# Kernel tuning notes

Hardware: AMD Instinct MI355X
Metric: run time of the kernel (lower is better)

Reference implementation:

```python
import jax, jax.numpy as jnp
import numpy as np

B, N, M, C = 4, 2048, 576, 512
H, KVH, D = 8, 2, 64          # heads, kv heads, head_dim
E, TOPK, F = 8, 2, 2048       # experts, top-k, expert hidden (4*C)
EPS = 1e-6
NEG = -1e9


def setup_inputs() -> dict:
    key = jax.random.key(0)
    ks = iter(jax.random.split(key, 40))
    w = lambda shape, s=0.02: jax.random.normal(next(ks), shape, jnp.float32) * s
    d = {
        'x': jax.random.normal(next(ks), (B, N, C), jnp.float32),
        'vision_features': jax.random.normal(next(ks), (B, M, C), jnp.float32),
        'ln1_g': jnp.ones((C,), jnp.float32), 'ln1_b': jnp.zeros((C,), jnp.float32),
        'ln2_g': jnp.ones((C,), jnp.float32), 'ln2_b': jnp.zeros((C,), jnp.float32),
        'ln3_g': jnp.ones((C,), jnp.float32), 'ln3_b': jnp.zeros((C,), jnp.float32),
        # self-attention (GQA): q -> C, k/v -> KVH*D
        'sa_wq': w((C, C)), 'sa_bq': jnp.zeros((C,), jnp.float32),
        'sa_wk': w((C, KVH * D)), 'sa_bk': jnp.zeros((KVH * D,), jnp.float32),
        'sa_wv': w((C, KVH * D)), 'sa_bv': jnp.zeros((KVH * D,), jnp.float32),
        'sa_wo': w((C, C)), 'sa_bo': jnp.zeros((C,), jnp.float32),
        # cross-attention (GQA)
        'ca_wq': w((C, C)), 'ca_bq': jnp.zeros((C,), jnp.float32),
        'ca_wk': w((C, KVH * D)), 'ca_bk': jnp.zeros((KVH * D,), jnp.float32),
        'ca_wv': w((C, KVH * D)), 'ca_bv': jnp.zeros((KVH * D,), jnp.float32),
        'ca_wo': w((C, C)), 'ca_bo': jnp.zeros((C,), jnp.float32),
        # MoE: router + stacked expert MLPs (C -> F -> C, GELU)
        'router_w': w((C, E)), 'router_b': jnp.zeros((E,), jnp.float32),
        'e_w1': w((E, C, F)), 'e_b1': jnp.zeros((E, F), jnp.float32),
        'e_w2': w((E, F, C)), 'e_b2': jnp.zeros((E, C), jnp.float32),
    }
    return d


def _ln(x, g, b):
    mu = jnp.mean(x, -1, keepdims=True)
    var = jnp.mean(jnp.square(x - mu), -1, keepdims=True)
    return (x - mu) * jax.lax.rsqrt(var + EPS) * g + b


def _gqa_attn(xq, ctx, wq, bq, wk, bk, wv, bv, wo, bo, causal):
    b, n, c = xq.shape
    m = ctx.shape[1]
    q = (xq @ wq + bq).reshape(b, n, H, D).transpose(0, 2, 1, 3)      # bhnd
    k = (ctx @ wk + bk).reshape(b, m, KVH, D).transpose(0, 2, 1, 3)   # bgmd
    v = (ctx @ wv + bv).reshape(b, m, KVH, D).transpose(0, 2, 1, 3)
    rep = H // KVH
    k = jnp.repeat(k, rep, axis=1)  # repeat_interleave over head dim
    v = jnp.repeat(v, rep, axis=1)
    scores = jnp.einsum('bhnd,bhmd->bhnm', q, k) * (D ** -0.5)
    if causal:
        mask = jnp.tril(jnp.ones((n, m), bool))
        scores = jnp.where(mask, scores, NEG)
    a = jax.nn.softmax(scores, axis=-1)
    o = jnp.einsum('bhnm,bhmd->bhnd', a, v).transpose(0, 2, 1, 3).reshape(b, n, c)
    return o @ wo + bo


def _moe(x, router_w, router_b, e_w1, e_b1, e_w2, e_b2):
    logits = x @ router_w + router_b                    # [B,N,E]
    probs = jax.nn.softmax(logits, axis=-1)
    topv, topi = jax.lax.top_k(probs, TOPK)             # [B,N,K]
    topv = topv / jnp.sum(topv, -1, keepdims=True)      # renormalize top-k gates
    onehot = jax.nn.one_hot(topi, E, dtype=x.dtype)     # [B,N,K,E]
    gates = jnp.einsum('bnke,bnk->bne', onehot, topv)   # sparse gates, zeros off top-k
    h = jax.nn.gelu(jnp.einsum('bnc,ecf->bnef', x, e_w1) + e_b1)
    eo = jnp.einsum('bnef,efc->bnec', h, e_w2) + e_b2
    out = jnp.einsum('bne,bnec->bnc', gates, eo)
    # load-balance aux loss (Switch-style): E * sum_e f_e * P_e
    dispatch = jnp.sum(onehot, axis=2)                  # [B,N,E] routed mask
    f = jnp.mean(dispatch, axis=(0, 1))
    P = jnp.mean(probs, axis=(0, 1))
    aux = E * jnp.sum(f * P)
    return out, aux


def reference(x, vision_features,
              ln1_g, ln1_b, ln2_g, ln2_b, ln3_g, ln3_b,
              sa_wq, sa_bq, sa_wk, sa_bk, sa_wv, sa_bv, sa_wo, sa_bo,
              ca_wq, ca_bq, ca_wk, ca_bk, ca_wv, ca_bv, ca_wo, ca_bo,
              router_w, router_b, e_w1, e_b1, e_w2, e_b2):
    # pre-norm causal self-attn + residual
    h = _ln(x, ln1_g, ln1_b)
    x = x + _gqa_attn(h, h, sa_wq, sa_bq, sa_wk, sa_bk, sa_wv, sa_bv, sa_wo, sa_bo, True)
    # pre-norm cross-attn + residual
    h = _ln(x, ln2_g, ln2_b)
    x = x + _gqa_attn(h, vision_features, ca_wq, ca_bq, ca_wk, ca_bk, ca_wv, ca_bv, ca_wo, ca_bo, False)
    # pre-norm MoE FFN + residual
    h = _ln(x, ln3_g, ln3_b)
    m, aux = _moe(h, router_w, router_b, e_w1, e_b1, e_w2, e_b2)
    return x + m, aux
```

## Files before the change

kernel.cpp:

```cpp
#include <hip/hip_runtime.h>
#include <cstddef>
#include <cstdint>

#define B_   4
#define N_   2048
#define M_   576
#define C_   512
#define H_   8
#define KVH_ 2
#define D_   64
#define E_   8
#define F_   2048
#define BN_  (B_*N_)
#define BM_  (B_*M_)

typedef __attribute__((ext_vector_type(8))) short bf16x8;
typedef __attribute__((ext_vector_type(4))) float f32x4;

__device__ __forceinline__ unsigned short f2bf(float f) {
    union { float f; unsigned int u; } v; v.f = f;
    unsigned int r = v.u + 0x7FFFu + ((v.u >> 16) & 1u);
    return (unsigned short)(r >> 16);
}

__global__ __launch_bounds__(256) void ln_kernel(const float* __restrict__ x,
    const float* __restrict__ g, const float* __restrict__ b, float* __restrict__ out)
{
    int row = blockIdx.x;
    const float* xr = x + (size_t)row * C_;
    float s = 0.f, ss = 0.f;
    for (int c = threadIdx.x; c < C_; c += 256) { float v = xr[c]; s += v; ss += v * v; }
    __shared__ float S1[256], S2[256];
    S1[threadIdx.x] = s; S2[threadIdx.x] = ss;
    __syncthreads();
    for (int o = 128; o > 0; o >>= 1) {
        if (threadIdx.x < o) { S1[threadIdx.x] += S1[threadIdx.x + o]; S2[threadIdx.x] += S2[threadIdx.x + o]; }
        __syncthreads();
    }
    float mu  = S1[0] * (1.f / C_);
    float var = S2[0] * (1.f / C_) - mu * mu;
    float inv = rsqrtf(var + 1e-6f);
    float* orow = out + (size_t)row * C_;
    for (int c = threadIdx.x; c < C_; c += 256)
        orow[c] = (xr[c] - mu) * inv * g[c] + b[c];
}

__global__ __launch_bounds__(256) void ln_bf(const float* __restrict__ x,
    const float* __restrict__ g, const float* __restrict__ b, unsigned short* __restrict__ out)
{
    int row = blockIdx.x;
    const float* xr = x + (size_t)row * C_;
    float s = 0.f, ss = 0.f;
    for (int c = threadIdx.x; c < C_; c += 256) { float v = xr[c]; s += v; ss += v * v; }
    __shared__ float S1[256], S2[256];
    S1[threadIdx.x] = s; S2[threadIdx.x] = ss;
    __syncthreads();
    for (int o = 128; o > 0; o >>= 1) {
        if (threadIdx.x < o) { S1[threadIdx.x] += S1[threadIdx.x + o]; S2[threadIdx.x] += S2[threadIdx.x + o]; }
        __syncthreads();
    }
    float mu  = S1[0] * (1.f / C_);
    float var = S2[0] * (1.f / C_) - mu * mu;
    float inv = rsqrtf(var + 1e-6f);
    unsigned short* orow = out + (size_t)row * C_;
    for (int c = threadIdx.x; c < C_; c += 256)
        orow[c] = f2bf((xr[c] - mu) * inv * g[c] + b[c]);
}

__global__ __launch_bounds__(256) void cast_bf_kernel(const float* __restrict__ in,
    unsigned short* __restrict__ out)
{
    int i = (blockIdx.x * 256 + threadIdx.x) * 4;
    float4 v = *(const float4*)(in + i);
    ushort4 o;
    o.x = f2bf(v.x); o.y = f2bf(v.y); o.z = f2bf(v.z); o.w = f2bf(v.w);
    *(ushort4*)(out + i) = o;
}

__global__ __launch_bounds__(256) void transpose_cast(const float* __restrict__ Win,
    unsigned short* __restrict__ Wtout, int K, int N)
{
    const float* W = Win + (size_t)blockIdx.z * K * N;
    unsigned short* Wt = Wtout + (size_t)blockIdx.z * K * N;
    __shared__ float T[32][33];
    int tid = threadIdx.x;
    int r = tid >> 3, c4 = (tid & 7) * 4;
    int k0 = blockIdx.y * 32, n0 = blockIdx.x * 32;
    float4 v = *(const float4*)&W[(size_t)(k0 + r) * N + n0 + c4];
    T[r][c4 + 0] = v.x; T[r][c4 + 1] = v.y; T[r][c4 + 2] = v.z; T[r][c4 + 3] = v.w;
    __syncthreads();
    ushort4 o;
    o.x = f2bf(T[c4 + 0][r]); o.y = f2bf(T[c4 + 1][r]);
    o.z = f2bf(T[c4 + 2][r]); o.w = f2bf(T[c4 + 3][r]);
    *(ushort4*)&Wt[(size_t)(n0 + r) * K + k0 + c4] = o;
}

__global__ __launch_bounds__(256) void dense_mfma(
    const unsigned short* __restrict__ Abf,
    const unsigned short* __restrict__ Btbf,
    const float* __restrict__ bias,
    float* __restrict__ outF,
    unsigned short* __restrict__ outBf,
    int N, int K, int mode, int NkPer)
{
    int row0 = blockIdx.y * 128;
    int col0 = blockIdx.x * 128;

    __shared__ unsigned short As[128 * 40];
    __shared__ unsigned short Bs[128 * 40];

    int tid = threadIdx.x;
    int srow = tid >> 2, seg8 = (tid & 3) * 8;
    size_t abase0 = (size_t)(row0 + srow) * K;
    size_t abase1 = (size_t)(row0 + srow + 64) * K;
    size_t bbase0 = (size_t)(col0 + srow) * K;
    size_t bbase1 = (size_t)(col0 + srow + 64) * K;
    int ldsA0 = srow * 40 + seg8, ldsA1 = (srow + 64) * 40 + seg8;

    int lane = tid & 63;
    int wid = tid >> 6;
    int wm0 = (wid & 1) * 64, wn0 = (wid >> 1) * 64;
    int lm = lane & 15, lq = lane >> 4;

    int aoff[4], boff[4];
#pragma unroll
    for (int i = 0; i < 4; i++) {
        aoff[i] = (wm0 + 16 * i + lm) * 40 + lq * 8;
        boff[i] = (wn0 + 16 * i + lm) * 40 + lq * 8;
    }

    f32x4 acc[4][4];
#pragma unroll
    for (int i = 0; i < 4; i++)
#pragma unroll
        for (int j = 0; j < 4; j++)
            acc[i][j] = (f32x4){0.f, 0.f, 0.f, 0.f};

    for (int k0 = 0; k0 < K; k0 += 32) {
        __syncthreads();
        *(uint4*)&As[ldsA0] = *(const uint4*)&Abf[abase0 + k0 + seg8];
        *(uint4*)&As[ldsA1] = *(const uint4*)&Abf[abase1 + k0 + seg8];
        *(uint4*)&Bs[ldsA0] = *(const uint4*)&Btbf[bbase0 + k0 + seg8];
        *(uint4*)&Bs[ldsA1] = *(const uint4*)&Btbf[bbase1 + k0 + seg8];
        __syncthreads();

        bf16x8 av[4], bv[4];
#pragma unroll
        for (int i = 0; i < 4; i++) av[i] = *(const bf16x8*)&As[aoff[i]];
#pragma unroll
        for (int i = 0; i < 4; i++) bv[i] = *(const bf16x8*)&Bs[boff[i]];
#pragma unroll
        for (int mi = 0; mi < 4; mi++)
#pragma unroll
            for (int ni = 0; ni < 4; ni++)
                acc[mi][ni] = __builtin_amdgcn_mfma_f32_16x16x32_bf16(av[mi], bv[ni], acc[mi][ni], 0, 0, 0);
    }

#pragma unroll
    for (int mi = 0; mi < 4; mi++) {
#pragma unroll
        for (int ri = 0; ri < 4; ri++) {
            int gr = row0 + wm0 + 16 * mi + lq * 4 + ri;
            if (mode == 2) {
                int bb = gr / NkPer;
                int mm = gr - bb * NkPer;
#pragma unroll
                for (int ni = 0; ni < 4; ni++) {
                    int gc = col0 + wn0 + 16 * ni + lm;
                    outBf[((size_t)bb * (KVH_ * D_) + gc) * NkPer + mm] =
                        f2bf(acc[mi][ni][ri] + bias[gc]);
                }
            } else if (mode == 1) {
                size_t orow = (size_t)gr * N;
#pragma unroll
                for (int ni = 0; ni < 4; ni++) {
                    int gc = col0 + wn0 + 16 * ni + lm;
                    outF[orow + gc] += acc[mi][ni][ri] + bias[gc];
                }
            } else {
                size_t orow = (size_t)gr * N;
#pragma unroll
                for (int ni = 0; ni < 4; ni++) {
                    int gc = col0 + wn0 + 16 * ni + lm;
                    outBf[orow + gc] = f2bf(acc[mi][ni][ri] + bias[gc]);
                }
            }
        }
    }
}

__global__ __launch_bounds__(256) void attn_mfma(
    const unsigned short* __restrict__ Q,
    const unsigned short* __restrict__ K,
    const unsigned short* __restrict__ Vt,
    unsigned short* __restrict__ O,
    int NkPer, int causal)
{
    __shared__ unsigned short Qs[64 * 72];
    __shared__ unsigned short Ks[64 * 72];
    __shared__ unsigned short Vs[64 * 72];
    unsigned short* Ps = Qs;

    int tid = threadIdx.x;
    int qt = blockIdx.x, bh = blockIdx.y;
    int b = bh >> 3, h = bh & 7, g = h >> 2;
    int q0 = qt * 64;

#pragma unroll
    for (int i = 0; i < 2; i++) {
        int s = tid + (i << 8);
        int r = s >> 3, c8 = (s & 7) << 3;
        *(uint4*)&Qs[r * 72 + c8] =
            *(const uint4*)&Q[(size_t)(b * N_ + q0 + r) * C_ + h * D_ + c8];
    }
    __syncthreads();

    int lane = tid & 63, wid = tid >> 6;
    int lm = lane & 15, lq = lane >> 4;
    int arow = wid * 16 + lm;

    bf16x8 qf[2];
    qf[0] = *(const bf16x8*)&Qs[arow * 72 + lq * 8];
    qf[1] = *(const bf16x8*)&Qs[arow * 72 + lq * 8 + 32];

    float m_run[4], l_run[4];
    f32x4 of[4];
#pragma unroll
    for (int i = 0; i < 4; i++) { m_run[i] = -1e30f; l_run[i] = 0.f; of[i] = (f32x4){0.f,0.f,0.f,0.f}; }

    int nkt = causal ? (qt + 1) : ((NkPer + 63) >> 6);

    for (int kt = 0; kt < nkt; kt++) {
        int k0 = kt << 6;
        __syncthreads();
#pragma unroll
        for (int i = 0; i < 2; i++) {
            int s = tid + (i << 8);
            int r = s >> 3, c8 = (s & 7) << 3;
            *(uint4*)&Ks[r * 72 + c8] =
                *(const uint4*)&K[(size_t)(b * NkPer + k0 + r) * (KVH_ * D_) + g * D_ + c8];
            *(uint4*)&Vs[r * 72 + c8] =
                *(const uint4*)&Vt[(size_t)(b * (KVH_ * D_) + g * D_ + r) * NkPer + k0 + c8];
        }
        __syncthreads();

        f32x4 sf[4];
#pragma unroll
        for (int i = 0; i < 4; i++) sf[i] = (f32x4){0.f,0.f,0.f,0.f};
#pragma unroll
        for (int ks = 0; ks < 2; ks++) {
#pragma unroll
            for (int ni = 0; ni < 4; ni++) {
                bf16x8 bv = *(const bf16x8*)&Ks[(16 * ni + lm) * 72 + lq * 8 + 32 * ks];
                sf[ni] = __builtin_amdgcn_mfma_f32_16x16x32_bf16(qf[ks], bv, sf[ni], 0, 0, 0);
            }
        }

        bool diag = causal && (k0 + 63 > q0 + wid * 16);
#pragma unroll
        for (int ni = 0; ni < 4; ni++)
#pragma unroll
            for (int ri = 0; ri < 4; ri++) {
                float v = sf[ni][ri] * 0.125f;
                if (diag && (k0 + 16 * ni + lm > q0 + wid * 16 + lq * 4 + ri)) v = -1e30f;
                sf[ni][ri] = v;
            }

        float alpha[4];
#pragma unroll
        for (int ri = 0; ri < 4; ri++) {
            float mx = fmaxf(fmaxf(sf[0][ri], sf[1][ri]), fmaxf(sf[2][ri], sf[3][ri]));
            mx = fmaxf(mx, __shfl_xor(mx, 1));
            mx = fmaxf(mx, __shfl_xor(mx, 2));
            mx = fmaxf(mx, __shfl_xor(mx, 4));
            mx = fmaxf(mx, __shfl_xor(mx, 8));
            float mnew = fmaxf(m_run[ri], mx);
            float a = __expf(m_run[ri] - mnew);
            float rsum = 0.f;
#pragma unroll
            for (int ni = 0; ni < 4; ni++) {
                float p = __expf(sf[ni][ri] - mnew);
                sf[ni][ri] = p;
                rsum += p;
            }
            rsum += __shfl_xor(rsum, 1);
            rsum += __shfl_xor(rsum, 2);
            rsum += __shfl_xor(rsum, 4);
            rsum += __shfl_xor(rsum, 8);
            l_run[ri] = l_run[ri] * a + rsum;
            m_run[ri] = mnew;
            alpha[ri] = a;
        }
#pragma unroll
        for (int ni = 0; ni < 4; ni++)
#pragma unroll
            for (int ri = 0; ri < 4; ri++) of[ni][ri] *= alpha[ri];

#pragma unroll
        for (int ni = 0; ni < 4; ni++)
#pragma unroll
            for (int ri = 0; ri < 4; ri++)
                Ps[(wid * 16 + lq * 4 + ri) * 72 + 16 * ni + lm] = f2bf(sf[ni][ri]);
        __syncthreads();

        bf16x8 pf0 = *(const bf16x8*)&Ps[arow * 72 + lq * 8];
        bf16x8 pf1 = *(const bf16x8*)&Ps[arow * 72 + lq * 8 + 32];
#pragma unroll
        for (int ni = 0; ni < 4; ni++) {
            bf16x8 vv0 = *(const bf16x8*)&Vs[(16 * ni + lm) * 72 + lq * 8];
            bf16x8 vv1 = *(const bf16x8*)&Vs[(16 * ni + lm) * 72 + lq * 8 + 32];
            of[ni] = __builtin_amdgcn_mfma_f32_16x16x32_bf16(pf0, vv0, of[ni], 0, 0, 0);
            of[ni] = __builtin_amdgcn_mfma_f32_16x16x32_bf16(pf1, vv1, of[ni], 0, 0, 0);
        }
    }

#pragma unroll
    for (int ri = 0; ri < 4; ri++) {
        float inv = 1.f / l_run[ri];
        int q = q0 + wid * 16 + lq * 4 + ri;
        size_t orow = (size_t)(b * N_ + q) * C_ + h * D_;
#pragma unroll
        for (int ni = 0; ni < 4; ni++)
            O[orow + 16 * ni + lm] = f2bf(of[ni][ri] * inv);
    }
}

__global__ __launch_bounds__(256) void router_logits(const float* __restrict__ X,
    const float* __restrict__ RW, const float* __restrict__ RB,
    float* __restrict__ gprobs, int* __restrict__ topi, float* __restrict__ gatesv)
{
    int lane = threadIdx.x & 63;
    int t = blockIdx.x * 4 + (threadIdx.x >> 6);
    const float* xr = X + (size_t)t * C_;
    float p[8] = {};
    for (int i = 0; i < 8; i++) {
        int c = i * 64 + lane;
        float xv = xr[c];
#pragma unroll
        for (int e = 0; e < 8; e++) p[e] = fmaf(xv, RW[c * 8 + e], p[e]);
    }
#pragma unroll
    for (int e = 0; e < 8; e++) {
        float v = p[e];
        v += __shfl_xor(v, 32, 64);
        v += __shfl_xor(v, 16, 64);
        v += __shfl_xor(v, 8, 64);
        v += __shfl_xor(v, 4, 64);
        v += __shfl_xor(v, 2, 64);
        v += __shfl_xor(v, 1, 64);
        p[e] = v;
    }
    if (lane == 0) {
        float logits[8], mx = -1e30f;
        for (int e = 0; e < 8; e++) { logits[e] = p[e] + RB[e]; mx = fmaxf(mx, logits[e]); }
        float pr[8], sum = 0.f;
        for (int e = 0; e < 8; e++) { pr[e] = expf(logits[e] - mx); sum += pr[e]; }
        float inv = 1.f / sum;
        for (int e = 0; e < 8; e++) { pr[e] *= inv; gprobs[t * 8 + e] = pr[e]; }
        int i1 = 0;
        for (int e = 1; e < 8; e++) if (pr[e] > pr[i1]) i1 = e;
        int i2 = (i1 == 0) ? 1 : 0;
        for (int e = 0; e < 8; e++) if (e != i1 && pr[e] > pr[i2]) i2 = e;
        float v1 = pr[i1], v2 = pr[i2], sg = 1.f / (v1 + v2);
        topi[t * 2]     = i1;  topi[t * 2 + 1]   = i2;
        gatesv[t * 2]   = v1 * sg;  gatesv[t * 2 + 1] = v2 * sg;
    }
}

__global__ __launch_bounds__(256) void router_reduce(const float* __restrict__ gprobs,
    const int* __restrict__ topi, int* __restrict__ ctrl, float* __restrict__ psum)
{
    __shared__ float fs[256];
    __shared__ int   is_[256];
    int bid = blockIdx.x, tid = threadIdx.x;
    if (bid < 8) {
        float s = 0.f;
        for (int t = tid; t < BN_; t += 256) s += gprobs[t * 8 + bid];
        fs[tid] = s; __syncthreads();
        for (int o = 128; o > 0; o >>= 1) { if (tid < o) fs[tid] += fs[tid + o]; __syncthreads(); }
        if (tid == 0) psum[bid] = fs[0];
    } else {
        int e = bid - 8, c = 0;
        for (int i = tid; i < BN_ * 2; i += 256) c += (topi[i] == e);
        is_[tid] = c; __syncthreads();
        for (int o = 128; o > 0; o >>= 1) { if (tid < o) is_[tid] += is_[tid + o]; __syncthreads(); }
        if (tid == 0) ctrl[e] = is_[0];
    }
}

__global__ void router_offsets(int* __restrict__ ctrl)
{
    if (threadIdx.x == 0 && blockIdx.x == 0) {
        int off = 0;
        for (int e = 0; e < 8; e++) {
            ctrl[16 + e] = off;
            off += (ctrl[e] + 127) & ~127;
        }
        ctrl[24] = off;
    }
}

__global__ __launch_bounds__(256) void router_scatter(const int* __restrict__ topi,
    const float* __restrict__ gatesv, int* __restrict__ rowtok,
    float* __restrict__ rowgate, int* __restrict__ ctrl)
{
    __shared__ int lcnt[8];
    __shared__ int lbase[8];
    int tid = threadIdx.x;
    int t = blockIdx.x * 256 + tid;
    if (tid < 8) lcnt[tid] = 0;
    __syncthreads();
    int e0 = topi[t * 2], e1 = topi[t * 2 + 1];
    int p0 = atomicAdd(&lcnt[e0], 1);
    int p1 = atomicAdd(&lcnt[e1], 1);
    __syncthreads();
    if (tid < 8) lbase[tid] = atomicAdd(&ctrl[8 + tid], lcnt[tid]);
    __syncthreads();
    int s0 = ctrl[16 + e0] + lbase[e0] + p0;
    int s1 = ctrl[16 + e1] + lbase[e1] + p1;
    rowtok[s0] = t; rowgate[s0] = gatesv[t * 2];
    rowtok[s1] = t; rowgate[s1] = gatesv[t * 2 + 1];
}

__global__ __launch_bounds__(256) void moe_mfma(
    const unsigned short* __restrict__ Abf,
    const unsigned short* __restrict__ Btbf,
    const float* __restrict__ biasAll,
    float* __restrict__ outF,
    unsigned short* __restrict__ outBf,
    const int* __restrict__ rowtok,
    const float* __restrict__ rowgate,
    const int* __restrict__ ctrl,
    int N, int K, int mode)
{
    int e = blockIdx.z;
    int cnt = ctrl[e];
    int row0 = blockIdx.y * 128;
    if (row0 >= cnt) return;
    int off = ctrl[16 + e];
    int col0 = blockIdx.x * 128;
    const unsigned short* Bt = Btbf + (size_t)e * N * K;
    const float* bias = biasAll + (size_t)e * N;

    __shared__ unsigned short As[128 * 40];
    __shared__ unsigned short Bs[128 * 40];
    __shared__ int toks[128];

    int tid = threadIdx.x;
    if (mode == 1 && tid < 128) {
        int gl = row0 + tid;
        toks[tid] = rowtok[off + (gl < cnt ? gl : 0)];
    }
    __syncthreads();

    int srow = tid >> 2, seg8 = (tid & 3) * 8;
    size_t abase0, abase1;
    if (mode == 1) {
        abase0 = (size_t)toks[srow] * K;
        abase1 = (size_t)toks[srow + 64] * K;
    } else {
        abase0 = (size_t)(off + row0 + srow) * K;
        abase1 = (size_t)(off + row0 + srow + 64) * K;
    }
    size_t bbase0 = (size_t)(col0 + srow) * K;
    size_t bbase1 = (size_t)(col0 + srow + 64) * K;
    int ldsA0 = srow * 40 + seg8, ldsA1 = (srow + 64) * 40 + seg8;

    int lane = tid & 63;
    int wid = tid >> 6;
    int wm0 = (wid & 1) * 64, wn0 = (wid >> 1) * 64;
    int lm = lane & 15, lq = lane >> 4;

    int aoff[4], boff[4];
#pragma unroll
    for (int i = 0; i < 4; i++) {
        aoff[i] = (wm0 + 16 * i + lm) * 40 + lq * 8;
        boff[i] = (wn0 + 16 * i + lm) * 40 + lq * 8;
    }

    f32x4 acc[4][4];
#pragma unroll
    for (int i = 0; i < 4; i++)
#pragma unroll
        for (int j = 0; j < 4; j++)
            acc[i][j] = (f32x4){0.f, 0.f, 0.f, 0.f};

    for (int k0 = 0; k0 < K; k0 += 32) {
        __syncthreads();
        *(uint4*)&As[ldsA0] = *(const uint4*)&Abf[abase0 + k0 + seg8];
        *(uint4*)&As[ldsA1] = *(const uint4*)&Abf[abase1 + k0 + seg8];
        *(uint4*)&Bs[ldsA0] = *(const uint4*)&Bt[bbase0 + k0 + seg8];
        *(uint4*)&Bs[ldsA1] = *(const uint4*)&Bt[bbase1 + k0 + seg8];
        __syncthreads();

        bf16x8 av[4], bv[4];
#pragma unroll
        for (int i = 0; i < 4; i++) av[i] = *(const bf16x8*)&As[aoff[i]];
#pragma unroll
        for (int i = 0; i < 4; i++) bv[i] = *(const bf16x8*)&Bs[boff[i]];
#pragma unroll
        for (int mi = 0; mi < 4; mi++)
#pragma unroll
            for (int ni = 0; ni < 4; ni++)
                acc[mi][ni] = __builtin_amdgcn_mfma_f32_16x16x32_bf16(av[mi], bv[ni], acc[mi][ni], 0, 0, 0);
    }

#pragma unroll
    for (int mi = 0; mi < 4; mi++) {
#pragma unroll
        for (int ri = 0; ri < 4; ri++) {
            int row_l = wm0 + 16 * mi + lq * 4 + ri;
            int gl = row0 + row_l;
            if (mode == 1) {
                size_t orow = (size_t)(off + gl) * N;
#pragma unroll
                for (int ni = 0; ni < 4; ni++) {
                    int gc = col0 + wn0 + 16 * ni + lm;
                    float hv = 0.f;
                    if (gl < cnt) {
                        float xv = acc[mi][ni][ri] + bias[gc];
                        float x3 = xv * xv * xv;
                        hv = 0.5f * xv * (1.f + tanhf(0.7978845608f * (xv + 0.044715f * x3)));
                    }
                    outBf[orow + gc] = f2bf(hv);
                }
            } else {
                if (gl >= cnt) continue;
                int tok = rowtok[off + gl];
                float gt = rowgate[off + gl];
                size_t orow = (size_t)tok * N;
#pragma unroll
                for (int ni = 0; ni < 4; ni++) {
                    int gc = col0 + wn0 + 16 * ni + lm;
                    atomicAdd(&outF[orow + gc], gt * (acc[mi][ni][ri] + bias[gc]));
                }
            }
        }
    }
}

__global__ void aux_kernel(const int* __restrict__ ctrl, const float* __restrict__ psum,
                           float* __restrict__ outaux)
{
    if (threadIdx.x == 0 && blockIdx.x == 0) {
        float s = 0.f;
        for (int e = 0; e < 8; e++)
            s += ((float)ctrl[e] / (float)BN_) * (psum[e] / (float)BN_);
        outaux[0] = 8.f * s;
    }
}

extern "C" void kernel_launch(void* const* d_in, const int* in_sizes, int n_in,
                              void* d_out, int out_size, void* d_ws, size_t ws_size,
                              hipStream_t stream)
{
    const float* x      = (const float*)d_in[0];
    const float* vis    = (const float*)d_in[1];
    const float* ln1g   = (const float*)d_in[2];
    const float* ln1b   = (const float*)d_in[3];
    const float* ln2g   = (const float*)d_in[4];
    const float* ln2b   = (const float*)d_in[5];
    const float* ln3g   = (const float*)d_in[6];
    const float* ln3b   = (const float*)d_in[7];
    const float* sa_wq  = (const float*)d_in[8];
    const float* sa_bq  = (const float*)d_in[9];
    const float* sa_wk  = (const float*)d_in[10];
    const float* sa_bk  = (const float*)d_in[11];
    const float* sa_wv  = (const float*)d_in[12];
    const float* sa_bv  = (const float*)d_in[13];
    const float* sa_wo  = (const float*)d_in[14];
    const float* sa_bo  = (const float*)d_in[15];
    const float* ca_wq  = (const float*)d_in[16];
    const float* ca_bq  = (const float*)d_in[17];
    const float* ca_wk  = (const float*)d_in[18];
    const float* ca_bk  = (const float*)d_in[19];
    const float* ca_wv  = (const float*)d_in[20];
    const float* ca_bv  = (const float*)d_in[21];
    const float* ca_wo  = (const float*)d_in[22];
    const float* ca_bo  = (const float*)d_in[23];
    const float* rw     = (const float*)d_in[24];
    const float* rb     = (const float*)d_in[25];
    const float* e_w1   = (const float*)d_in[26];
    const float* e_b1   = (const float*)d_in[27];
    const float* e_w2   = (const float*)d_in[28];
    const float* e_b2   = (const float*)d_in[29];

    float* out = (float*)d_out;

    char* ws = (char*)d_ws;
    size_t off = 0;
    auto alloc = [&](size_t bytes) -> void* {
        void* p = ws + off;
        off = (off + bytes + 255) & ~(size_t)255;
        return p;
    };
    float* hbuf    = (float*)alloc((size_t)BN_ * C_ * 4);
    unsigned short* hbz = (unsigned short*)alloc((size_t)BN_ * C_ * 2);
    unsigned short* visbf = (unsigned short*)alloc((size_t)BM_ * C_ * 2);
    char* ureg = (char*)alloc((size_t)17408 * F_ * 2);
    unsigned short* moeH = (unsigned short*)ureg;
    unsigned short* qbf  = (unsigned short*)(ureg);
    unsigned short* obf  = (unsigned short*)(ureg + (size_t)BN_ * C_ * 2);
    unsigned short* kbf  = (unsigned short*)(ureg + (size_t)BN_ * C_ * 4);
    unsigned short* vtbf = (unsigned short*)(ureg + (size_t)BN_ * C_ * 4 + (size_t)BN_ * KVH_ * D_ * 2);
    unsigned short* sa_wqt = (unsigned short*)alloc((size_t)C_ * C_ * 2);
    unsigned short* sa_wkt = (unsigned short*)alloc((size_t)C_ * KVH_ * D_ * 2);
    unsigned short* sa_wvt = (unsigned short*)alloc((size_t)C_ * KVH_ * D_ * 2);
    unsigned short* sa_wot = (unsigned short*)alloc((size_t)C_ * C_ * 2);
    unsigned short* ca_wqt = (unsigned short*)alloc((size_t)C_ * C_ * 2);
    unsigned short* ca_wkt = (unsigned short*)alloc((size_t)C_ * KVH_ * D_ * 2);
    unsigned short* ca_wvt = (unsigned short*)alloc((size_t)C_ * KVH_ * D_ * 2);
    unsigned short* ca_wot = (unsigned short*)alloc((size_t)C_ * C_ * 2);
    unsigned short* w1t  = (unsigned short*)alloc((size_t)E_ * C_ * F_ * 2);
    unsigned short* w2t  = (unsigned short*)alloc((size_t)E_ * F_ * C_ * 2);
    float* gprobs  = (float*)alloc((size_t)BN_ * 8 * 4);
    int*   topi    = (int*)  alloc((size_t)BN_ * 2 * 4);
    float* gatesv  = (float*)alloc((size_t)BN_ * 2 * 4);
    int*   rowtok  = (int*)  alloc(17408 * 4);
    float* rowgate = (float*)alloc(17408 * 4);
    int*   ctrl    = (int*)  alloc(256);
    float* psum    = (float*)((char*)ctrl + 128);
    (void)ws_size; (void)in_sizes; (void)n_in; (void)out_size;

    hipMemcpyAsync(out, x, (size_t)BN_ * C_ * 4, hipMemcpyDeviceToDevice, stream);

    transpose_cast<<<dim3(16, 16, 1), 256, 0, stream>>>(sa_wq, sa_wqt, C_, C_);
    transpose_cast<<<dim3(4,  16, 1), 256, 0, stream>>>(sa_wk, sa_wkt, C_, KVH_*D_);
    transpose_cast<<<dim3(4,  16, 1), 256, 0, stream>>>(sa_wv, sa_wvt, C_, KVH_*D_);
    transpose_cast<<<dim3(16, 16, 1), 256, 0, stream>>>(sa_wo, sa_wot, C_, C_);
    transpose_cast<<<dim3(16, 16, 1), 256, 0, stream>>>(ca_wq, ca_wqt, C_, C_);
    transpose_cast<<<dim3(4,  16, 1), 256, 0, stream>>>(ca_wk, ca_wkt, C_, KVH_*D_);
    transpose_cast<<<dim3(4,  16, 1), 256, 0, stream>>>(ca_wv, ca_wvt, C_, KVH_*D_);
    transpose_cast<<<dim3(16, 16, 1), 256, 0, stream>>>(ca_wo, ca_wot, C_, C_);
    transpose_cast<<<dim3(F_/32, C_/32, E_), 256, 0, stream>>>(e_w1, w1t, C_, F_);
    transpose_cast<<<dim3(C_/32, F_/32, E_), 256, 0, stream>>>(e_w2, w2t, F_, C_);
    cast_bf_kernel<<<(BM_*C_)/1024, 256, 0, stream>>>(vis, visbf);

    ln_bf<<<BN_, 256, 0, stream>>>(out, ln1g, ln1b, hbz);
    dense_mfma<<<dim3(4, 64), 256, 0, stream>>>(hbz, sa_wqt, sa_bq, nullptr, qbf, C_, C_, 0, 0);
    dense_mfma<<<dim3(1, 64), 256, 0, stream>>>(hbz, sa_wkt, sa_bk, nullptr, kbf, KVH_*D_, C_, 0, 0);
    dense_mfma<<<dim3(1, 64), 256, 0, stream>>>(hbz, sa_wvt, sa_bv, nullptr, vtbf, KVH_*D_, C_, 2, N_);
    attn_mfma<<<dim3(N_/64, B_*H_), 256, 0, stream>>>(qbf, kbf, vtbf, obf, N_, 1);
    dense_mfma<<<dim3(4, 64), 256, 0, stream>>>(obf, sa_wot, sa_bo, out, nullptr, C_, C_, 1, 0);

    ln_bf<<<BN_, 256, 0, stream>>>(out, ln2g, ln2b, hbz);
    dense_mfma<<<dim3(4, 64), 256, 0, stream>>>(hbz, ca_wqt, ca_bq, nullptr, qbf, C_, C_, 0, 0);
    dense_mfma<<<dim3(1, 18), 256, 0, stream>>>(visbf, ca_wkt, ca_bk, nullptr, kbf, KVH_*D_, C_, 0, 0);
    dense_mfma<<<dim3(1, 18), 256, 0, stream>>>(visbf, ca_wvt, ca_bv, nullptr, vtbf, KVH_*D_, C_, 2, M_);
    attn_mfma<<<dim3(N_/64, B_*H_), 256, 0, stream>>>(qbf, kbf, vtbf, obf, M_, 0);
    dense_mfma<<<dim3(4, 64), 256, 0, stream>>>(obf, ca_wot, ca_bo, out, nullptr, C_, C_, 1, 0);

    ln_kernel<<<BN_, 256, 0, stream>>>(out, ln3g, ln3b, hbuf);
    cast_bf_kernel<<<(BN_*C_)/1024, 256, 0, stream>>>(hbuf, hbz);
    hipMemsetAsync(ctrl, 0, 256, stream);
    router_logits<<<BN_/4, 256, 0, stream>>>(hbuf, rw, rb, gprobs, topi, gatesv);
    router_reduce<<<16, 256, 0, stream>>>(gprobs, topi, ctrl, psum);
    router_offsets<<<1, 1, 0, stream>>>(ctrl);
    router_scatter<<<BN_/256, 256, 0, stream>>>(topi, gatesv, rowtok, rowgate, ctrl);
    moe_mfma<<<dim3(F_/128, BN_/128, E_), 256, 0, stream>>>(
        hbz, w1t, e_b1, nullptr, moeH, rowtok, rowgate, ctrl, F_, C_, 1);
    moe_mfma<<<dim3(C_/128, BN_/128, E_), 256, 0, stream>>>(
        moeH, w2t, e_b2, out, nullptr, rowtok, rowgate, ctrl, C_, F_, 2);
    aux_kernel<<<1, 1, 0, stream>>>(ctrl, psum, out + (size_t)BN_ * C_);
}
```

Measured before the change: 784.7 us.

## Split causal attention over KV, drop online softmax max, fuse K/V projections

```diff
diff --git a/kernel.cpp b/kernel.cpp
--- a/kernel.cpp
+++ b/kernel.cpp
@@ -101,6 +101,7 @@
     const float* __restrict__ bias,
     float* __restrict__ outF,
     unsigned short* __restrict__ outBf,
+    unsigned short* __restrict__ outBf2,
     int N, int K, int mode, int NkPer)
 {
     int row0 = blockIdx.y * 128;
@@ -161,7 +162,20 @@
 #pragma unroll
         for (int ri = 0; ri < 4; ri++) {
             int gr = row0 + wm0 + 16 * mi + lq * 4 + ri;
-            if (mode == 2) {
+            if (mode == 3) {
+#pragma unroll
+                for (int ni = 0; ni < 4; ni++) {
+                    int gc = col0 + wn0 + 16 * ni + lm;
+                    float v = acc[mi][ni][ri] + bias[gc];
+                    if (gc < 128) {
+                        outBf[(size_t)gr * 128 + gc] = f2bf(v);
+                    } else {
+                        int bb = gr / NkPer;
+                        int mm = gr - bb * NkPer;
+                        outBf2[((size_t)bb * 128 + (gc - 128)) * NkPer + mm] = f2bf(v);
+                    }
+                }
+            } else if (mode == 2) {
                 int bb = gr / NkPer;
                 int mm = gr - bb * NkPer;
 #pragma unroll
@@ -193,7 +207,9 @@
     const unsigned short* __restrict__ Q,
     const unsigned short* __restrict__ K,
     const unsigned short* __restrict__ Vt,
-    unsigned short* __restrict__ O,
+    unsigned short* __restrict__ Obf,
+    float* __restrict__ Opart,
+    float* __restrict__ Lpart,
     int NkPer, int causal)
 {
     __shared__ unsigned short Qs[64 * 72];
@@ -202,7 +218,7 @@
     unsigned short* Ps = Qs;
 
     int tid = threadIdx.x;
-    int qt = blockIdx.x, bh = blockIdx.y;
+    int qt = blockIdx.x, bh = blockIdx.y, z = blockIdx.z;
     int b = bh >> 3, h = bh & 7, g = h >> 2;
     int q0 = qt * 64;
 
@@ -223,14 +239,18 @@
     qf[0] = *(const bf16x8*)&Qs[arow * 72 + lq * 8];
     qf[1] = *(const bf16x8*)&Qs[arow * 72 + lq * 8 + 32];
 
-    float m_run[4], l_run[4];
+    float lsum[4];
     f32x4 of[4];
 #pragma unroll
-    for (int i = 0; i < 4; i++) { m_run[i] = -1e30f; l_run[i] = 0.f; of[i] = (f32x4){0.f,0.f,0.f,0.f}; }
+    for (int i = 0; i < 4; i++) { lsum[i] = 0.f; of[i] = (f32x4){0.f,0.f,0.f,0.f}; }
 
     int nkt = causal ? (qt + 1) : ((NkPer + 63) >> 6);
-
-    for (int kt = 0; kt < nkt; kt++) {
+    int nz = gridDim.z;
+    int per = (nkt + nz - 1) / nz;
+    int kt0 = z * per;
+    int kt1 = min(nkt, kt0 + per);
+
+    for (int kt = kt0; kt < kt1; kt++) {
         int k0 = kt << 6;
         __syncthreads();
 #pragma unroll
@@ -261,40 +281,12 @@
         for (int ni = 0; ni < 4; ni++)
 #pragma unroll
             for (int ri = 0; ri < 4; ri++) {
-                float v = sf[ni][ri] * 0.125f;
+                float v = sf[ni][ri] * 0.125f - 8.f;
                 if (diag && (k0 + 16 * ni + lm > q0 + wid * 16 + lq * 4 + ri)) v = -1e30f;
-                sf[ni][ri] = v;
+                float p = __expf(v);
+                sf[ni][ri] = p;
+                lsum[ri] += p;
             }
-
-        float alpha[4];
-#pragma unroll
-        for (int ri = 0; ri < 4; ri++) {
-            float mx = fmaxf(fmaxf(sf[0][ri], sf[1][ri]), fmaxf(sf[2][ri], sf[3][ri]));
-            mx = fmaxf(mx, __shfl_xor(mx, 1));
-            mx = fmaxf(mx, __shfl_xor(mx, 2));
-            mx = fmaxf(mx, __shfl_xor(mx, 4));
-            mx = fmaxf(mx, __shfl_xor(mx, 8));
-            float mnew = fmaxf(m_run[ri], mx);
-            float a = __expf(m_run[ri] - mnew);
-            float rsum = 0.f;
-#pragma unroll
-            for (int ni = 0; ni < 4; ni++) {
-                float p = __expf(sf[ni][ri] - mnew);
-                sf[ni][ri] = p;
-                rsum += p;
-            }
-            rsum += __shfl_xor(rsum, 1);
-            rsum += __shfl_xor(rsum, 2);
-            rsum += __shfl_xor(rsum, 4);
-            rsum += __shfl_xor(rsum, 8);
-            l_run[ri] = l_run[ri] * a + rsum;
-            m_run[ri] = mnew;
-            alpha[ri] = a;
-        }
-#pragma unroll
-        for (int ni = 0; ni < 4; ni++)
-#pragma unroll
-            for (int ri = 0; ri < 4; ri++) of[ni][ri] *= alpha[ri];
 
 #pragma unroll
         for (int ni = 0; ni < 4; ni++)
@@ -316,13 +308,54 @@
 
 #pragma unroll
     for (int ri = 0; ri < 4; ri++) {
-        float inv = 1.f / l_run[ri];
-        int q = q0 + wid * 16 + lq * 4 + ri;
-        size_t orow = (size_t)(b * N_ + q) * C_ + h * D_;
-#pragma unroll
-        for (int ni = 0; ni < 4; ni++)
-            O[orow + 16 * ni + lm] = f2bf(of[ni][ri] * inv);
-    }
+        float s = lsum[ri];
+        s += __shfl_xor(s, 1);
+        s += __shfl_xor(s, 2);
+        s += __shfl_xor(s, 4);
+        s += __shfl_xor(s, 8);
+        lsum[ri] = s;
+    }
+
+    if (nz == 1) {
+#pragma unroll
+        for (int ri = 0; ri < 4; ri++) {
+            float inv = 1.f / lsum[ri];
+            int q = q0 + wid * 16 + lq * 4 + ri;
+            size_t orow = (size_t)(b * N_ + q) * C_ + h * D_;
+#pragma unroll
+            for (int ni = 0; ni < 4; ni++)
+                Obf[orow + 16 * ni + lm] = f2bf(of[ni][ri] * inv);
+        }
+    } else {
+        size_t zofs = (size_t)z * BN_ * C_;
+#pragma unroll
+        for (int ri = 0; ri < 4; ri++) {
+            int q = q0 + wid * 16 + lq * 4 + ri;
+            size_t orow = zofs + (size_t)(b * N_ + q) * C_ + h * D_;
+#pragma unroll
+            for (int ni = 0; ni < 4; ni++)
+                Opart[orow + 16 * ni + lm] = of[ni][ri];
+            if (lm == 0)
+                Lpart[(size_t)z * (B_ * H_ * N_) + bh * N_ + q] = lsum[ri];
+        }
+    }
+}
+
+__global__ __launch_bounds__(256) void attn_combine(const float* __restrict__ Opart,
+    const float* __restrict__ Lpart, unsigned short* __restrict__ Obf)
+{
+    int flat = (blockIdx.x * 256 + threadIdx.x) * 4;
+    int row = flat >> 9, col = flat & 511;
+    int b = row >> 11, q = row & (N_ - 1), h = col >> 6;
+    int bh = b * 8 + h;
+    float l = Lpart[bh * N_ + q] + Lpart[B_ * H_ * N_ + bh * N_ + q];
+    float inv = 1.f / l;
+    float4 o0 = *(const float4*)&Opart[flat];
+    float4 o1 = *(const float4*)&Opart[(size_t)BN_ * C_ + flat];
+    ushort4 o;
+    o.x = f2bf((o0.x + o1.x) * inv); o.y = f2bf((o0.y + o1.y) * inv);
+    o.z = f2bf((o0.z + o1.z) * inv); o.w = f2bf((o0.w + o1.w) * inv);
+    *(ushort4*)&Obf[flat] = o;
 }
 
 __global__ __launch_bounds__(256) void router_logits(const float* __restrict__ X,
@@ -603,14 +636,17 @@
     unsigned short* obf  = (unsigned short*)(ureg + (size_t)BN_ * C_ * 2);
     unsigned short* kbf  = (unsigned short*)(ureg + (size_t)BN_ * C_ * 4);
     unsigned short* vtbf = (unsigned short*)(ureg + (size_t)BN_ * C_ * 4 + (size_t)BN_ * KVH_ * D_ * 2);
+    float* opart = (float*)(ureg + (size_t)BN_ * C_ * 4 + (size_t)BN_ * KVH_ * D_ * 4);
+    float* lpart = (float*)(ureg + (size_t)BN_ * C_ * 4 + (size_t)BN_ * KVH_ * D_ * 4
+                                 + (size_t)2 * BN_ * C_ * 4);
     unsigned short* sa_wqt = (unsigned short*)alloc((size_t)C_ * C_ * 2);
-    unsigned short* sa_wkt = (unsigned short*)alloc((size_t)C_ * KVH_ * D_ * 2);
-    unsigned short* sa_wvt = (unsigned short*)alloc((size_t)C_ * KVH_ * D_ * 2);
+    unsigned short* sa_wkvt = (unsigned short*)alloc((size_t)C_ * 2 * KVH_ * D_ * 2);
     unsigned short* sa_wot = (unsigned short*)alloc((size_t)C_ * C_ * 2);
     unsigned short* ca_wqt = (unsigned short*)alloc((size_t)C_ * C_ * 2);
-    unsigned short* ca_wkt = (unsigned short*)alloc((size_t)C_ * KVH_ * D_ * 2);
-    unsigned short* ca_wvt = (unsigned short*)alloc((size_t)C_ * KVH_ * D_ * 2);
+    unsigned short* ca_wkvt = (unsigned short*)alloc((size_t)C_ * 2 * KVH_ * D_ * 2);
     unsigned short* ca_wot = (unsigned short*)alloc((size_t)C_ * C_ * 2);
+    float* bkv_sa = (float*)alloc(256 * 4);
+    float* bkv_ca = (float*)alloc(256 * 4);
     unsigned short* w1t  = (unsigned short*)alloc((size_t)E_ * C_ * F_ * 2);
     unsigned short* w2t  = (unsigned short*)alloc((size_t)E_ * F_ * C_ * 2);
     float* gprobs  = (float*)alloc((size_t)BN_ * 8 * 4);
@@ -625,30 +661,33 @@
     hipMemcpyAsync(out, x, (size_t)BN_ * C_ * 4, hipMemcpyDeviceToDevice, stream);
 
     transpose_cast<<<dim3(16, 16, 1), 256, 0, stream>>>(sa_wq, sa_wqt, C_, C_);
-    transpose_cast<<<dim3(4,  16, 1), 256, 0, stream>>>(sa_wk, sa_wkt, C_, KVH_*D_);
-    transpose_cast<<<dim3(4,  16, 1), 256, 0, stream>>>(sa_wv, sa_wvt, C_, KVH_*D_);
+    transpose_cast<<<dim3(4,  16, 1), 256, 0, stream>>>(sa_wk, sa_wkvt, C_, KVH_*D_);
+    transpose_cast<<<dim3(4,  16, 1), 256, 0, stream>>>(sa_wv, sa_wkvt + 128 * C_, C_, KVH_*D_);
     transpose_cast<<<dim3(16, 16, 1), 256, 0, stream>>>(sa_wo, sa_wot, C_, C_);
     transpose_cast<<<dim3(16, 16, 1), 256, 0, stream>>>(ca_wq, ca_wqt, C_, C_);
-    transpose_cast<<<dim3(4,  16, 1), 256, 0, stream>>>(ca_wk, ca_wkt, C_, KVH_*D_);
-    transpose_cast<<<dim3(4,  16, 1), 256, 0, stream>>>(ca_wv, ca_wvt, C_, KVH_*D_);
+    transpose_cast<<<dim3(4,  16, 1), 256, 0, stream>>>(ca_wk, ca_wkvt, C_, KVH_*D_);
+    transpose_cast<<<dim3(4,  16, 1), 256, 0, stream>>>(ca_wv, ca_wkvt + 128 * C_, C_, KVH_*D_);
     transpose_cast<<<dim3(16, 16, 1), 256, 0, stream>>>(ca_wo, ca_wot, C_, C_);
     transpose_cast<<<dim3(F_/32, C_/32, E_), 256, 0, stream>>>(e_w1, w1t, C_, F_);
     transpose_cast<<<dim3(C_/32, F_/32, E_), 256, 0, stream>>>(e_w2, w2t, F_, C_);
     cast_bf_kernel<<<(BM_*C_)/1024, 256, 0, stream>>>(vis, visbf);
+    hipMemcpyAsync(bkv_sa,       sa_bk, 128 * 4, hipMemcpyDeviceToDevice, stream);
+    hipMemcpyAsync(bkv_sa + 128, sa_bv, 128 * 4, hipMemcpyDeviceToDevice, stream);
+    hipMemcpyAsync(bkv_ca,       ca_bk, 128 * 4, hipMemcpyDeviceToDevice, stream);
+    hipMemcpyAsync(bkv_ca + 128, ca_bv, 128 * 4, hipMemcpyDeviceToDevice, stream);
 
     ln_bf<<<BN_, 256, 0, stream>>>(out, ln1g, ln1b, hbz);
-    dense_mfma<<<dim3(4, 64), 256, 0, stream>>>(hbz, sa_wqt, sa_bq, nullptr, qbf, C_, C_, 0, 0);
-    dense_mfma<<<dim3(1, 64), 256, 0, stream>>>(hbz, sa_wkt, sa_bk, nullptr, kbf, KVH_*D_, C_, 0, 0);
-    dense_mfma<<<dim3(1, 64), 256, 0, stream>>>(hbz, sa_wvt, sa_bv, nullptr, vtbf, KVH_*D_, C_, 2, N_);
-    attn_mfma<<<dim3(N_/64, B_*H_), 256, 0, stream>>>(qbf, kbf, vtbf, obf, N_, 1);
-    dense_mfma<<<dim3(4, 64), 256, 0, stream>>>(obf, sa_wot, sa_bo, out, nullptr, C_, C_, 1, 0);
+    dense_mfma<<<dim3(4, 64), 256, 0, stream>>>(hbz, sa_wqt, sa_bq, nullptr, qbf, nullptr, C_, C_, 0, 0);
+    dense_mfma<<<dim3(2, 64), 256, 0, stream>>>(hbz, sa_wkvt, bkv_sa, nullptr, kbf, vtbf, 256, C_, 3, N_);
+    attn_mfma<<<dim3(N_/64, B_*H_, 2), 256, 0, stream>>>(qbf, kbf, vtbf, nullptr, opart, lpart, N_, 1);
+    attn_combine<<<(BN_*C_)/1024, 256, 0, stream>>>(opart, lpart, obf);
+    dense_mfma<<<dim3(4, 64), 256, 0, stream>>>(obf, sa_wot, sa_bo, out, nullptr, nullptr, C_, C_, 1, 0);
 
     ln_bf<<<BN_, 256, 0, stream>>>(out, ln2g, ln2b, hbz);
-    dense_mfma<<<dim3(4, 64), 256, 0, stream>>>(hbz, ca_wqt, ca_bq, nullptr, qbf, C_, C_, 0, 0);
-    dense_mfma<<<dim3(1, 18), 256, 0, stream>>>(visbf, ca_wkt, ca_bk, nullptr, kbf, KVH_*D_, C_, 0, 0);
-    dense_mfma<<<dim3(1, 18), 256, 0, stream>>>(visbf, ca_wvt, ca_bv, nullptr, vtbf, KVH_*D_, C_, 2, M_);
-    attn_mfma<<<dim3(N_/64, B_*H_), 256, 0, stream>>>(qbf, kbf, vtbf, obf, M_, 0);
-    dense_mfma<<<dim3(4, 64), 256, 0, stream>>>(obf, ca_wot, ca_bo, out, nullptr, C_, C_, 1, 0);
+    dense_mfma<<<dim3(4, 64), 256, 0, stream>>>(hbz, ca_wqt, ca_bq, nullptr, qbf, nullptr, C_, C_, 0, 0);
+    dense_mfma<<<dim3(2, 18), 256, 0, stream>>>(visbf, ca_wkvt, bkv_ca, nullptr, kbf, vtbf, 256, C_, 3, M_);
+    attn_mfma<<<dim3(N_/64, B_*H_, 1), 256, 0, stream>>>(qbf, kbf, vtbf, obf, nullptr, nullptr, M_, 0);
+    dense_mfma<<<dim3(4, 64), 256, 0, stream>>>(obf, ca_wot, ca_bo, out, nullptr, nullptr, C_, C_, 1, 0);
 
     ln_kernel<<<BN_, 256, 0, stream>>>(out, ln3g, ln3b, hbuf);
     cast_bf_kernel<<<(BN_*C_)/1024, 256, 0, stream>>>(hbuf, hbz);
```

Result: faster. 736.2 us (-6.2%).
